# Kernel tuning notes

Hardware: AMD Instinct MI355X
Metric: run time of the kernel (lower is better)

The kernel has to match this reference:

```python
import jax, jax.numpy as jnp
import numpy as np

LEAKY_SLOPE = 0.01  # torch nn.LeakyReLU default
N, K, D = 50000, 32, 128


def setup_inputs() -> dict:
    key = jax.random.key(0)
    k1, k2, k3 = jax.random.split(key, 3)
    feat = jax.random.normal(k1, (N, D), dtype=jnp.float32)
    sele_nei = jax.random.randint(k2, (N, K), 0, N)
    # xavier_normal with gain=1.414 on shape (1, 2D): std = gain*sqrt(2/(1+2D))
    std = 1.414 * np.sqrt(2.0 / (1 + 2 * D))
    att = jax.random.normal(k3, (1, 2 * D), dtype=jnp.float32) * std
    return {"feat": feat, "sele_nei": sele_nei, "att": att}


def reference(feat, sele_nei, att):
    # nei_emb = feat[sele_nei]: [N, K, D] gather
    nei_emb = feat[sele_nei]
    # score = leakyrelu(concat([h_refer, nei_emb], -1) @ att.T)
    # split att to avoid materializing the [N, K, 2D] concat:
    a_ref = att[0, :D]   # [D]
    a_nei = att[0, D:]   # [D]
    score_ref = feat @ a_ref                      # [N]
    score_nei = jnp.einsum('nkd,d->nk', nei_emb, a_nei)  # [N, K]
    score = score_ref[:, None] + score_nei        # [N, K]
    score = jnp.where(score >= 0, score, LEAKY_SLOPE * score)
    w = jax.nn.softmax(score, axis=1)             # softmax over neighbors
    out = jnp.einsum('nk,nkd->nd', w, nei_emb)    # weighted sum over K
    return jax.nn.elu(out)                        # [N, D]
```

## Files before the change

### kernel.cpp

```cpp
#include <hip/hip_runtime.h>
#include <hip/hip_fp16.h>
#include <math.h>

#define N_NODES 50000
#define K_NEI   32
#define D_FEAT  128
#define LEAKY   0.01f

#define NPG  2
#define GPB  8
#define NPB  (NPG * GPB)
#define GRID (N_NODES / NPB)

#define CHUNK_SHIFT 12
#define NCHUNKS     ((N_NODES + (1 << CHUNK_SHIFT) - 1) >> CHUNK_SHIFT)

__global__ __launch_bounds__(256) void precompute_kernel(
    const float* __restrict__ feat,
    const float* __restrict__ att,
    unsigned short* __restrict__ fh,
    float* __restrict__ g,
    float* __restrict__ h)
{
    const int lane = threadIdx.x & 31;
    const int row  = blockIdx.x * 8 + (threadIdx.x >> 5);
    if (row >= N_NODES) return;

    const float4 a_ref = *(const float4*)&att[4 * lane];
    const float4 a_nei = *(const float4*)&att[D_FEAT + 4 * lane];
    const float4 f     = *(const float4*)&feat[(size_t)row * D_FEAT + 4 * lane];

    float sr = f.x * a_ref.x + f.y * a_ref.y + f.z * a_ref.z + f.w * a_ref.w;
    float sn = f.x * a_nei.x + f.y * a_nei.y + f.z * a_nei.z + f.w * a_nei.w;
    #pragma unroll
    for (int off = 16; off >= 1; off >>= 1) {
        sr += __shfl_xor(sr, off, 32);
        sn += __shfl_xor(sn, off, 32);
    }
    if (lane == 0) { h[row] = sr; g[row] = sn; }

    const __half2 p0 = __floats2half2_rn(f.x, f.y);
    const __half2 p1 = __floats2half2_rn(f.z, f.w);
    uint2 st;
    st.x = *(const unsigned*)&p0;
    st.y = *(const unsigned*)&p1;
    *(uint2*)&fh[(size_t)row * D_FEAT + 4 * lane] = st;
}

__global__ __launch_bounds__(256, 8) void gather_lds(
    const unsigned short* __restrict__ fh,
    const int*   __restrict__ nei,
    const float* __restrict__ g,
    const float* __restrict__ h,
    float*       __restrict__ out)
{
    __shared__ uint4 pairs4[GPB][K_NEI];

    const int lane       = threadIdx.x & 31;
    const int grp        = threadIdx.x >> 5;
    const int group      = blockIdx.x * GPB + grp;
    const int half_shift = threadIdx.x & 32;
    const int node0      = group * NPG;
    const unsigned lt    = (1u << lane) - 1u;

    #pragma unroll
    for (int j = 0; j < NPG; ++j) {
        const int node = node0 + j;

        const int idx = nei[node * K_NEI + lane];
        float sc = h[node] + g[idx];
        sc = (sc >= 0.f) ? sc : LEAKY * sc;
        const float p = __expf(sc);
        float denom = p;
        #pragma unroll
        for (int off = 16; off >= 1; off >>= 1)
            denom += __shfl_xor(denom, off, 32);
        const float w = p / denom;

        const int cid = idx >> CHUNK_SHIFT;
        int rank = 0;
        #pragma unroll
        for (int c = 0; c < NCHUNKS; ++c) {
            const unsigned long long b = __ballot(cid == c);
            const unsigned bh = (unsigned)(b >> half_shift);
            rank += (c < cid)  ? __popc(bh)      : 0;
            rank += (c == cid) ? __popc(bh & lt) : 0;
        }
        ((uint2*)&pairs4[grp][rank])[j] = make_uint2((unsigned)idx, __float_as_uint(w));
    }
    __syncthreads();

    const int hl  = lane & 15;
    const int sel = (lane >> 4) & 1;

    float4 olo = make_float4(0.f, 0.f, 0.f, 0.f);
    float4 ohi = make_float4(0.f, 0.f, 0.f, 0.f);

    const char* fbase = (const char*)fh;
    const unsigned lbyte = (unsigned)(hl << 4);

    #pragma unroll 8
    for (int i = 0; i < K_NEI; ++i) {
        const uint4 t = pairs4[grp][i];
        const unsigned ridx = sel ? t.z : t.x;
        const float    wk   = __uint_as_float(sel ? t.w : t.y);
        const uint4 v = *(const uint4*)(fbase + ((ridx << 8) + lbyte));

        const __half2 h0 = *(const __half2*)&v.x;
        const __half2 h1 = *(const __half2*)&v.y;
        const __half2 h2 = *(const __half2*)&v.z;
        const __half2 h3 = *(const __half2*)&v.w;
        olo.x += wk * __half2float(h0.x);
        olo.y += wk * __half2float(h0.y);
        olo.z += wk * __half2float(h1.x);
        olo.w += wk * __half2float(h1.y);
        ohi.x += wk * __half2float(h2.x);
        ohi.y += wk * __half2float(h2.y);
        ohi.z += wk * __half2float(h3.x);
        ohi.w += wk * __half2float(h3.y);
    }

    const int node = node0 + sel;
    float4 r0, r1;
    r0.x = (olo.x > 0.f) ? olo.x : (__expf(olo.x) - 1.f);
    r0.y = (olo.y > 0.f) ? olo.y : (__expf(olo.y) - 1.f);
    r0.z = (olo.z > 0.f) ? olo.z : (__expf(olo.z) - 1.f);
    r0.w = (olo.w > 0.f) ? olo.w : (__expf(olo.w) - 1.f);
    r1.x = (ohi.x > 0.f) ? ohi.x : (__expf(ohi.x) - 1.f);
    r1.y = (ohi.y > 0.f) ? ohi.y : (__expf(ohi.y) - 1.f);
    r1.z = (ohi.z > 0.f) ? ohi.z : (__expf(ohi.z) - 1.f);
    r1.w = (ohi.w > 0.f) ? ohi.w : (__expf(ohi.w) - 1.f);

    float* op = &out[(size_t)node * D_FEAT + hl * 8];
    *(float4*)op       = r0;
    *(float4*)(op + 4) = r1;
}

__global__ __launch_bounds__(256, 4) void feat_encoder_fallback(
    const float* __restrict__ feat,
    const int*   __restrict__ nei,
    const float* __restrict__ att,
    float*       __restrict__ out)
{
    const int lane = threadIdx.x & 31;
    const int node = blockIdx.x * 8 + (threadIdx.x >> 5);
    if (node >= N_NODES) return;

    const float4 a_ref = *(const float4*)&att[4 * lane];
    const float4 a_nei = *(const float4*)&att[D_FEAT + 4 * lane];

    const float4 f = *(const float4*)&feat[(size_t)node * D_FEAT + 4 * lane];
    float sref = f.x * a_ref.x + f.y * a_ref.y + f.z * a_ref.z + f.w * a_ref.w;
    #pragma unroll
    for (int off = 16; off >= 1; off >>= 1)
        sref += __shfl_xor(sref, off, 32);

    const int idx = nei[node * K_NEI + lane];
    float  s = 0.f;
    float4 o = {0.f, 0.f, 0.f, 0.f};
    #pragma unroll
    for (int k = 0; k < K_NEI; ++k) {
        const int nk = __shfl(idx, k, 32);
        const float4 v = *(const float4*)&feat[(size_t)nk * D_FEAT + 4 * lane];
        float partial = v.x * a_nei.x + v.y * a_nei.y + v.z * a_nei.z + v.w * a_nei.w;
        #pragma unroll
        for (int off = 16; off >= 1; off >>= 1)
            partial += __shfl_xor(partial, off, 32);
        float score = partial + sref;
        score = (score >= 0.f) ? score : LEAKY * score;
        const float p = __expf(score);
        s += p;
        o.x += p * v.x; o.y += p * v.y; o.z += p * v.z; o.w += p * v.w;
    }
    const float inv = 1.0f / s;
    float4 r;
    r.x = o.x * inv; r.y = o.y * inv; r.z = o.z * inv; r.w = o.w * inv;
    r.x = (r.x > 0.f) ? r.x : expm1f(r.x);
    r.y = (r.y > 0.f) ? r.y : expm1f(r.y);
    r.z = (r.z > 0.f) ? r.z : expm1f(r.z);
    r.w = (r.w > 0.f) ? r.w : expm1f(r.w);
    *(float4*)&out[(size_t)node * D_FEAT + 4 * lane] = r;
}

extern "C" void kernel_launch(void* const* d_in, const int* in_sizes, int n_in,
                              void* d_out, int out_size, void* d_ws, size_t ws_size,
                              hipStream_t stream) {
    const float* feat = (const float*)d_in[0];
    const int*   nei  = (const int*)d_in[1];
    const float* att  = (const float*)d_in[2];
    float*       out  = (float*)d_out;

    const size_t fh_bytes = (size_t)N_NODES * D_FEAT * sizeof(unsigned short);
    const size_t g_bytes  = (size_t)N_NODES * sizeof(float);
    const size_t need     = fh_bytes + 2 * g_bytes;

    if (ws_size >= need) {
        unsigned short* fh = (unsigned short*)d_ws;
        float* g = (float*)((char*)d_ws + fh_bytes);
        float* h = (float*)((char*)d_ws + fh_bytes + g_bytes);
        precompute_kernel<<<dim3((N_NODES + 7) / 8), 256, 0, stream>>>(feat, att, fh, g, h);
        gather_lds<<<dim3(GRID), 256, 0, stream>>>(fh, nei, g, h, out);
    } else {
        feat_encoder_fallback<<<dim3((N_NODES + 7) / 8), 256, 0, stream>>>(feat, nei, att, out);
    }
}
```

Measured before the change: 54.41 us.

## Process four nodes per group with software-pipelined gather loads and no block barrier

Each 32-lane group now handles four nodes instead of two, keeping the neighbor pairs in two LDS tables. The main loop keeps eight 16-byte feature row loads in flight through a manual rotating prefetch. The block-level barrier is dropped because each group only reads LDS entries it wrote itself within one wave. Launch bounds drop to four blocks per CU to allow more registers, and bounds checks are added for the now non-divisible grid. This trades occupancy for more memory-level parallelism per wave.

```diff
diff --git a/kernel.cpp b/kernel.cpp
--- a/kernel.cpp
+++ b/kernel.cpp
@@ -7,10 +7,10 @@
 #define D_FEAT  128
 #define LEAKY   0.01f
 
-#define NPG  2
+#define NPG  4
 #define GPB  8
 #define NPB  (NPG * GPB)
-#define GRID (N_NODES / NPB)
+#define GRID ((N_NODES + NPB - 1) / NPB)
 
 #define CHUNK_SHIFT 12
 #define NCHUNKS     ((N_NODES + (1 << CHUNK_SHIFT) - 1) >> CHUNK_SHIFT)
@@ -47,14 +47,43 @@
     *(uint2*)&fh[(size_t)row * D_FEAT + 4 * lane] = st;
 }
 
-__global__ __launch_bounds__(256, 8) void gather_lds(
+__device__ __forceinline__ void acc8(float4& oLo, float4& oHi, float wgt, uint4 v) {
+    const __half2 h0 = *(const __half2*)&v.x;
+    const __half2 h1 = *(const __half2*)&v.y;
+    const __half2 h2 = *(const __half2*)&v.z;
+    const __half2 h3 = *(const __half2*)&v.w;
+    oLo.x += wgt * __half2float(h0.x);
+    oLo.y += wgt * __half2float(h0.y);
+    oLo.z += wgt * __half2float(h1.x);
+    oLo.w += wgt * __half2float(h1.y);
+    oHi.x += wgt * __half2float(h2.x);
+    oHi.y += wgt * __half2float(h2.y);
+    oHi.z += wgt * __half2float(h3.x);
+    oHi.w += wgt * __half2float(h3.y);
+}
+
+#define FETCHA(slot, rank) do { \
+    const uint4 t_ = pA[(rank)]; \
+    w##slot = __uint_as_float(sel ? t_.w : t_.y); \
+    v##slot = *(const uint4*)(fbase + (((sel ? t_.z : t_.x) << 8) + lbyte)); \
+} while (0)
+#define FETCHB(slot, rank) do { \
+    const uint4 t_ = pB[(rank)]; \
+    w##slot = __uint_as_float(sel ? t_.w : t_.y); \
+    v##slot = *(const uint4*)(fbase + (((sel ? t_.z : t_.x) << 8) + lbyte)); \
+} while (0)
+#define CONSA(slot) acc8(aLo, aHi, w##slot, v##slot)
+#define CONSB(slot) acc8(bLo, bHi, w##slot, v##slot)
+
+__global__ __launch_bounds__(256, 4) void gather_lds(
     const unsigned short* __restrict__ fh,
     const int*   __restrict__ nei,
     const float* __restrict__ g,
     const float* __restrict__ h,
     float*       __restrict__ out)
 {
-    __shared__ uint4 pairs4[GPB][K_NEI];
+    __shared__ uint4 pairsA[GPB][K_NEI];
+    __shared__ uint4 pairsB[GPB][K_NEI];
 
     const int lane       = threadIdx.x & 31;
     const int grp        = threadIdx.x >> 5;
@@ -65,17 +94,18 @@
 
     #pragma unroll
     for (int j = 0; j < NPG; ++j) {
-        const int node = node0 + j;
-
-        const int idx = nei[node * K_NEI + lane];
-        float sc = h[node] + g[idx];
+        const int  node  = node0 + j;
+        const bool valid = (node < N_NODES);
+
+        const int idx = valid ? nei[node * K_NEI + lane] : 0;
+        float sc = valid ? (h[node] + g[idx]) : 0.f;
         sc = (sc >= 0.f) ? sc : LEAKY * sc;
         const float p = __expf(sc);
         float denom = p;
         #pragma unroll
         for (int off = 16; off >= 1; off >>= 1)
             denom += __shfl_xor(denom, off, 32);
-        const float w = p / denom;
+        const float w = valid ? (p / denom) : 0.f;
 
         const int cid = idx >> CHUNK_SHIFT;
         int rank = 0;
@@ -86,54 +116,74 @@
             rank += (c < cid)  ? __popc(bh)      : 0;
             rank += (c == cid) ? __popc(bh & lt) : 0;
         }
-        ((uint2*)&pairs4[grp][rank])[j] = make_uint2((unsigned)idx, __float_as_uint(w));
-    }
-    __syncthreads();
+        if (j < 2) ((uint2*)&pairsA[grp][rank])[j]     = make_uint2((unsigned)idx, __float_as_uint(w));
+        else       ((uint2*)&pairsB[grp][rank])[j - 2] = make_uint2((unsigned)idx, __float_as_uint(w));
+    }
 
     const int hl  = lane & 15;
     const int sel = (lane >> 4) & 1;
 
-    float4 olo = make_float4(0.f, 0.f, 0.f, 0.f);
-    float4 ohi = make_float4(0.f, 0.f, 0.f, 0.f);
+    float4 aLo = make_float4(0.f, 0.f, 0.f, 0.f);
+    float4 aHi = make_float4(0.f, 0.f, 0.f, 0.f);
+    float4 bLo = make_float4(0.f, 0.f, 0.f, 0.f);
+    float4 bHi = make_float4(0.f, 0.f, 0.f, 0.f);
 
     const char* fbase = (const char*)fh;
     const unsigned lbyte = (unsigned)(hl << 4);
-
-    #pragma unroll 8
-    for (int i = 0; i < K_NEI; ++i) {
-        const uint4 t = pairs4[grp][i];
-        const unsigned ridx = sel ? t.z : t.x;
-        const float    wk   = __uint_as_float(sel ? t.w : t.y);
-        const uint4 v = *(const uint4*)(fbase + ((ridx << 8) + lbyte));
-
-        const __half2 h0 = *(const __half2*)&v.x;
-        const __half2 h1 = *(const __half2*)&v.y;
-        const __half2 h2 = *(const __half2*)&v.z;
-        const __half2 h3 = *(const __half2*)&v.w;
-        olo.x += wk * __half2float(h0.x);
-        olo.y += wk * __half2float(h0.y);
-        olo.z += wk * __half2float(h1.x);
-        olo.w += wk * __half2float(h1.y);
-        ohi.x += wk * __half2float(h2.x);
-        ohi.y += wk * __half2float(h2.y);
-        ohi.z += wk * __half2float(h3.x);
-        ohi.w += wk * __half2float(h3.y);
-    }
-
-    const int node = node0 + sel;
+    const uint4* pA = &pairsA[grp][0];
+    const uint4* pB = &pairsB[grp][0];
+
+    uint4 v0, v1, v2, v3, v4, v5, v6, v7;
+    float w0, w1, w2, w3, w4, w5, w6, w7;
+
+    FETCHA(0, 0); FETCHB(1, 0); FETCHA(2, 1); FETCHB(3, 1);
+    FETCHA(4, 2); FETCHB(5, 2); FETCHA(6, 3); FETCHB(7, 3);
+
+    #pragma unroll 1
+    for (int i = 0; i < 2 * K_NEI - 8; i += 8) {
+        CONSA(0); FETCHA(0, (i + 8)  >> 1);
+        CONSB(1); FETCHB(1, (i + 8)  >> 1);
+        CONSA(2); FETCHA(2, (i + 10) >> 1);
+        CONSB(3); FETCHB(3, (i + 10) >> 1);
+        CONSA(4); FETCHA(4, (i + 12) >> 1);
+        CONSB(5); FETCHB(5, (i + 12) >> 1);
+        CONSA(6); FETCHA(6, (i + 14) >> 1);
+        CONSB(7); FETCHB(7, (i + 14) >> 1);
+    }
+    CONSA(0); CONSB(1); CONSA(2); CONSB(3);
+    CONSA(4); CONSB(5); CONSA(6); CONSB(7);
+
+    const int nodeA = node0 + sel;
+    const int nodeB = node0 + 2 + sel;
     float4 r0, r1;
-    r0.x = (olo.x > 0.f) ? olo.x : (__expf(olo.x) - 1.f);
-    r0.y = (olo.y > 0.f) ? olo.y : (__expf(olo.y) - 1.f);
-    r0.z = (olo.z > 0.f) ? olo.z : (__expf(olo.z) - 1.f);
-    r0.w = (olo.w > 0.f) ? olo.w : (__expf(olo.w) - 1.f);
-    r1.x = (ohi.x > 0.f) ? ohi.x : (__expf(ohi.x) - 1.f);
-    r1.y = (ohi.y > 0.f) ? ohi.y : (__expf(ohi.y) - 1.f);
-    r1.z = (ohi.z > 0.f) ? ohi.z : (__expf(ohi.z) - 1.f);
-    r1.w = (ohi.w > 0.f) ? ohi.w : (__expf(ohi.w) - 1.f);
-
-    float* op = &out[(size_t)node * D_FEAT + hl * 8];
-    *(float4*)op       = r0;
-    *(float4*)(op + 4) = r1;
+
+    r0.x = (aLo.x > 0.f) ? aLo.x : (__expf(aLo.x) - 1.f);
+    r0.y = (aLo.y > 0.f) ? aLo.y : (__expf(aLo.y) - 1.f);
+    r0.z = (aLo.z > 0.f) ? aLo.z : (__expf(aLo.z) - 1.f);
+    r0.w = (aLo.w > 0.f) ? aLo.w : (__expf(aLo.w) - 1.f);
+    r1.x = (aHi.x > 0.f) ? aHi.x : (__expf(aHi.x) - 1.f);
+    r1.y = (aHi.y > 0.f) ? aHi.y : (__expf(aHi.y) - 1.f);
+    r1.z = (aHi.z > 0.f) ? aHi.z : (__expf(aHi.z) - 1.f);
+    r1.w = (aHi.w > 0.f) ? aHi.w : (__expf(aHi.w) - 1.f);
+    if (nodeA < N_NODES) {
+        float* op = &out[(size_t)nodeA * D_FEAT + hl * 8];
+        *(float4*)op       = r0;
+        *(float4*)(op + 4) = r1;
+    }
+
+    r0.x = (bLo.x > 0.f) ? bLo.x : (__expf(bLo.x) - 1.f);
+    r0.y = (bLo.y > 0.f) ? bLo.y : (__expf(bLo.y) - 1.f);
+    r0.z = (bLo.z > 0.f) ? bLo.z : (__expf(bLo.z) - 1.f);
+    r0.w = (bLo.w > 0.f) ? bLo.w : (__expf(bLo.w) - 1.f);
+    r1.x = (bHi.x > 0.f) ? bHi.x : (__expf(bHi.x) - 1.f);
+    r1.y = (bHi.y > 0.f) ? bHi.y : (__expf(bHi.y) - 1.f);
+    r1.z = (bHi.z > 0.f) ? bHi.z : (__expf(bHi.z) - 1.f);
+    r1.w = (bHi.w > 0.f) ? bHi.w : (__expf(bHi.w) - 1.f);
+    if (nodeB < N_NODES) {
+        float* op = &out[(size_t)nodeB * D_FEAT + hl * 8];
+        *(float4*)op       = r0;
+        *(float4*)(op + 4) = r1;
+    }
 }
 
 __global__ __launch_bounds__(256, 4) void feat_encoder_fallback(
```

After: 62.25 us. 1.14x slower.

## Add software L2 prefetch of half-precision feature table and drop block barrier

Applied to the files above, without the earlier changes.

Each thread issues dummy 16-byte loads that sweep 1 MB strides of the fp16 feature table. The results are kept live only through empty inline asm, so the gathered neighbour rows should already sit in cache. The loads are interleaved between four unrolled 8-neighbour accumulation segments. The __syncthreads between writing the per-group neighbour/weight pairs to LDS and reading them back is removed. That relies on each group's pairs being written and read within the same wavefront. The extra loads add a large amount of redundant memory traffic and VGPR pressure, and dropping the barrier risks LDS ordering problems.

```diff
diff --git a/kernel.cpp b/kernel.cpp
--- a/kernel.cpp
+++ b/kernel.cpp
@@ -14,6 +14,7 @@
 
 #define CHUNK_SHIFT 12
 #define NCHUNKS     ((N_NODES + (1 << CHUNK_SHIFT) - 1) >> CHUNK_SHIFT)
+#define FH_CLAMP    (N_NODES * D_FEAT * 2 - 16)
 
 __global__ __launch_bounds__(256) void precompute_kernel(
     const float* __restrict__ feat,
@@ -47,6 +48,32 @@
     *(uint2*)&fh[(size_t)row * D_FEAT + 4 * lane] = st;
 }
 
+#define PF(slot, c) do { \
+    unsigned a_ = ((unsigned)(c) << 20) + pfoff; \
+    a_ = (a_ > (unsigned)FH_CLAMP) ? (unsigned)FH_CLAMP : a_; \
+    slot = *(const uint4*)(fbase + a_); \
+} while (0)
+#define PFUSE(slot) asm volatile("" :: "v"(slot.x), "v"(slot.y), "v"(slot.z), "v"(slot.w))
+
+#define BODY(i) do { \
+    const uint4 t_ = pairs4[grp][(i)];             \
+    const unsigned ridx_ = sel ? t_.z : t_.x; \
+    const float    wk_   = __uint_as_float(sel ? t_.w : t_.y); \
+    const uint4 v_ = *(const uint4*)(fbase + ((ridx_ << 8) + lbyte)); \
+    const __half2 h0_ = *(const __half2*)&v_.x; \
+    const __half2 h1_ = *(const __half2*)&v_.y; \
+    const __half2 h2_ = *(const __half2*)&v_.z; \
+    const __half2 h3_ = *(const __half2*)&v_.w; \
+    olo.x += wk_ * __half2float(h0_.x); \
+    olo.y += wk_ * __half2float(h0_.y); \
+    olo.z += wk_ * __half2float(h1_.x); \
+    olo.w += wk_ * __half2float(h1_.y); \
+    ohi.x += wk_ * __half2float(h2_.x); \
+    ohi.y += wk_ * __half2float(h2_.y); \
+    ohi.z += wk_ * __half2float(h3_.x); \
+    ohi.w += wk_ * __half2float(h3_.y); \
+} while (0)
+
 __global__ __launch_bounds__(256, 8) void gather_lds(
     const unsigned short* __restrict__ fh,
     const int*   __restrict__ nei,
@@ -62,6 +89,12 @@
     const int half_shift = threadIdx.x & 32;
     const int node0      = group * NPG;
     const unsigned lt    = (1u << lane) - 1u;
+
+    const char* fbase = (const char*)fh;
+    const unsigned pfoff = (((blockIdx.x >> 3) << 12) + (threadIdx.x << 4)) & 0xFFFFFu;
+
+    uint4 pf0, pf1, pf2, pf3;
+    PF(pf0, 0); PF(pf1, 1); PF(pf2, 2); PF(pf3, 3);
 
     #pragma unroll
     for (int j = 0; j < NPG; ++j) {
@@ -88,7 +121,6 @@
         }
         ((uint2*)&pairs4[grp][rank])[j] = make_uint2((unsigned)idx, __float_as_uint(w));
     }
-    __syncthreads();
 
     const int hl  = lane & 15;
     const int sel = (lane >> 4) & 1;
@@ -96,29 +128,23 @@
     float4 olo = make_float4(0.f, 0.f, 0.f, 0.f);
     float4 ohi = make_float4(0.f, 0.f, 0.f, 0.f);
 
-    const char* fbase = (const char*)fh;
     const unsigned lbyte = (unsigned)(hl << 4);
 
-    #pragma unroll 8
-    for (int i = 0; i < K_NEI; ++i) {
-        const uint4 t = pairs4[grp][i];
-        const unsigned ridx = sel ? t.z : t.x;
-        const float    wk   = __uint_as_float(sel ? t.w : t.y);
-        const uint4 v = *(const uint4*)(fbase + ((ridx << 8) + lbyte));
-
-        const __half2 h0 = *(const __half2*)&v.x;
-        const __half2 h1 = *(const __half2*)&v.y;
-        const __half2 h2 = *(const __half2*)&v.z;
-        const __half2 h3 = *(const __half2*)&v.w;
-        olo.x += wk * __half2float(h0.x);
-        olo.y += wk * __half2float(h0.y);
-        olo.z += wk * __half2float(h1.x);
-        olo.w += wk * __half2float(h1.y);
-        ohi.x += wk * __half2float(h2.x);
-        ohi.y += wk * __half2float(h2.y);
-        ohi.z += wk * __half2float(h3.x);
-        ohi.w += wk * __half2float(h3.y);
-    }
+    #pragma unroll
+    for (int i = 0; i < 8; ++i) BODY(i);
+    PFUSE(pf0); PF(pf0, 4); PFUSE(pf1); PF(pf1, 5); PFUSE(pf2); PF(pf2, 6);
+
+    #pragma unroll
+    for (int i = 8; i < 16; ++i) BODY(i);
+    PFUSE(pf3); PF(pf3, 7); PFUSE(pf0); PF(pf0, 8); PFUSE(pf1); PF(pf1, 9);
+
+    #pragma unroll
+    for (int i = 16; i < 24; ++i) BODY(i);
+    PFUSE(pf2); PF(pf2, 10); PFUSE(pf3); PF(pf3, 11); PFUSE(pf0); PF(pf0, 12);
+
+    #pragma unroll
+    for (int i = 24; i < 32; ++i) BODY(i);
+    PFUSE(pf0); PFUSE(pf1); PFUSE(pf2); PFUSE(pf3);
 
     const int node = node0 + sel;
     float4 r0, r1;
```

New measurement: 96.98 us. +78.3%, slower.
